# Kernel tuning notes

Hardware: AMD Instinct MI355X
Metric: run time of the kernel (lower is better)

The kernel has to match this reference:

```python
import jax, jax.numpy as jnp
import numpy as np

NUM_NODES = 100_000
NUM_EDGES = 3_200_000
NUM_GRAPHS = 200
F_IN = 128
HID = 64
BN_EPS = 1e-5


def setup_inputs() -> dict:
    key = jax.random.key(0)
    ks = jax.random.split(key, 12)
    x = jax.random.normal(ks[0], (NUM_NODES, F_IN), dtype=jnp.float32)
    edge_index = jax.random.randint(ks[1], (2, NUM_EDGES), 0, NUM_NODES, dtype=jnp.int64)
    batch = jnp.sort(jax.random.randint(ks[2], (NUM_NODES,), 0, NUM_GRAPHS, dtype=jnp.int64))
    s1 = float(np.sqrt(6.0 / F_IN))  # kaiming_uniform-ish bound
    s2 = float(np.sqrt(6.0 / HID))
    W1 = jax.random.uniform(ks[3], (HID, F_IN), jnp.float32, -s1, s1)
    b1 = jnp.zeros((HID,), jnp.float32)
    W2 = jax.random.uniform(ks[4], (HID, HID), jnp.float32, -s2, s2)
    b2 = jnp.zeros((HID,), jnp.float32)
    gamma1 = jnp.ones((HID,), jnp.float32)
    beta1 = jnp.zeros((HID,), jnp.float32)
    mean1 = 0.1 * jax.random.normal(ks[5], (HID,), jnp.float32)
    var1 = jax.random.uniform(ks[6], (HID,), jnp.float32, 0.5, 1.5)
    gamma2 = jnp.ones((HID,), jnp.float32)
    beta2 = jnp.zeros((HID,), jnp.float32)
    mean2 = 0.1 * jax.random.normal(ks[7], (HID,), jnp.float32)
    var2 = jax.random.uniform(ks[8], (HID,), jnp.float32, 0.5, 1.5)
    Wl = jax.random.uniform(ks[9], (1, HID), jnp.float32, -s2, s2)
    bl = jnp.zeros((1,), jnp.float32)
    return dict(x=x, edge_index=edge_index, batch=batch,
                W1=W1, b1=b1, gamma1=gamma1, beta1=beta1, mean1=mean1, var1=var1,
                W2=W2, b2=b2, gamma2=gamma2, beta2=beta2, mean2=mean2, var2=var2,
                Wl=Wl, bl=bl)


def _gcn_conv(x, W, b, src, dst, dinv):
    # PyG GCNConv: h = x @ W.T, then D^{-1/2}(A+I)D^{-1/2} aggregation, then + bias
    h = x @ W.T                                    # [N, out]
    w_edge = (dinv[src] * dinv[dst])[:, None]      # [E, 1]
    msg = h[src] * w_edge                          # [E, out] gather
    agg = jax.ops.segment_sum(msg, dst, num_segments=NUM_NODES)
    agg = agg + h * (dinv * dinv)[:, None]         # self-loop term
    return agg + b


def _bn_eval(h, gamma, beta, mean, var):
    return (h - mean) * (gamma * jax.lax.rsqrt(var + BN_EPS)) + beta


def reference(x, edge_index, batch,
              W1, b1, gamma1, beta1, mean1, var1,
              W2, b2, gamma2, beta2, mean2, var2,
              Wl, bl):
    src, dst = edge_index[0], edge_index[1]
    # degrees over A + I (self-loops add 1)
    deg = jax.ops.segment_sum(jnp.ones((NUM_EDGES,), jnp.float32), dst,
                              num_segments=NUM_NODES) + 1.0
    dinv = jax.lax.rsqrt(deg)
    h = jax.nn.relu(_bn_eval(_gcn_conv(x, W1, b1, src, dst, dinv),
                             gamma1, beta1, mean1, var1))
    # dropout = identity (eval mode)
    h = jax.nn.relu(_bn_eval(_gcn_conv(h, W2, b2, src, dst, dinv),
                             gamma2, beta2, mean2, var2))
    # global_mean_pool over graph ids
    sums = jax.ops.segment_sum(h, batch, num_segments=NUM_GRAPHS)
    cnts = jax.ops.segment_sum(jnp.ones((NUM_NODES,), jnp.float32), batch,
                               num_segments=NUM_GRAPHS)
    pooled = sums / jnp.maximum(cnts, 1.0)[:, None]  # [G, 64]
    return pooled @ Wl.T + bl                        # [G, 1]
```

## Files before the change

### kernel.cpp

```cpp
#include <hip/hip_runtime.h>
#include <hip/hip_bf16.h>

#define NN 100000
#define FF 128
#define HH 64
#define BN_EPS 1e-5f

typedef unsigned int uint_t;

__device__ __forceinline__ float bflo(uint_t u) { return __uint_as_float(u << 16); }
__device__ __forceinline__ float bfhi(uint_t u) { return __uint_as_float(u & 0xFFFF0000u); }
__device__ __forceinline__ unsigned short f2bf(float f) {
    uint_t a = __float_as_uint(f); a += 0x7FFF + ((a >> 16) & 1); return (unsigned short)(a >> 16);
}
__device__ __forceinline__ uint_t f2bf2(float lo, float hi) {
    uint_t a = __float_as_uint(lo); a += 0x7FFF + ((a >> 16) & 1);
    uint_t b = __float_as_uint(hi); b += 0x7FFF + ((b >> 16) & 1);
    return (a >> 16) | (b & 0xFFFF0000u);
}

__global__ void k_detect(const unsigned* __restrict__ ei, int* __restrict__ flag) {
    if (threadIdx.x == 0 && blockIdx.x == 0) {
        unsigned o = 0;
        for (int i = 1; i < 32; i += 2) o |= ei[i];
        *flag = (o == 0) ? 1 : 0;
    }
}

__device__ __forceinline__ int load_idx(const void* p, int i, int is64) {
    return is64 ? (int)((const long long*)p)[i] : ((const int*)p)[i];
}

__global__ void k_count(const void* __restrict__ ei, int E, const int* __restrict__ flag,
                        int* __restrict__ counts) {
    int e = blockIdx.x * blockDim.x + threadIdx.x;
    if (e >= E) return;
    int is64 = *flag;
    int d = load_idx(ei, E + e, is64);
    atomicAdd(&counts[d], 1);
}

__global__ void k_dinv(const int* __restrict__ counts, float* __restrict__ dinv,
                       const void* __restrict__ bat, const int* __restrict__ flag,
                       int* __restrict__ gcnt, int N) {
    int i = blockIdx.x * blockDim.x + threadIdx.x;
    if (i >= N) return;
    float deg = (float)counts[i] + 1.0f;
    dinv[i] = rsqrtf(deg);
    int is64 = *flag;
    int b = load_idx(bat, i, is64);
    atomicAdd(&gcnt[b], 1);
}

__global__ void k_scan1(const int* __restrict__ counts, int* __restrict__ partial, int N) {
    __shared__ int s[512];
    int t = threadIdx.x;
    int i = blockIdx.x * 512 + t;
    int v = (i < N) ? counts[i] : 0;
    s[t] = v; __syncthreads();
    for (int off = 256; off; off >>= 1) {
        if (t < off) s[t] += s[t + off];
        __syncthreads();
    }
    if (t == 0) partial[blockIdx.x] = s[0];
}

__global__ void k_scan2(int* __restrict__ partial, int nch) {
    __shared__ int s[256];
    int t = threadIdx.x;
    int v = (t < nch) ? partial[t] : 0;
    s[t] = v; __syncthreads();
    for (int off = 1; off < 256; off <<= 1) {
        int add = (t >= off) ? s[t - off] : 0;
        __syncthreads();
        s[t] += add;
        __syncthreads();
    }
    if (t < nch) partial[t] = s[t] - v;
}

__global__ void k_scan3(const int* __restrict__ counts, const int* __restrict__ partial,
                        int* __restrict__ rp, int N, int E) {
    __shared__ int s[512];
    int t = threadIdx.x;
    int i = blockIdx.x * 512 + t;
    int v = (i < N) ? counts[i] : 0;
    s[t] = v; __syncthreads();
    for (int off = 1; off < 512; off <<= 1) {
        int add = (t >= off) ? s[t - off] : 0;
        __syncthreads();
        s[t] += add;
        __syncthreads();
    }
    if (i < N) rp[i] = partial[blockIdx.x] + s[t] - v;
    if (i == N) rp[N] = E;
}

__global__ void k_fill(const void* __restrict__ ei, int E, const int* __restrict__ flag,
                       const float* __restrict__ dinv, const int* __restrict__ rp,
                       int* __restrict__ fillcnt, int2* __restrict__ cw) {
    int e = blockIdx.x * blockDim.x + threadIdx.x;
    if (e >= E) return;
    int is64 = *flag;
    int s = load_idx(ei, e, is64);
    int d = load_idx(ei, E + e, is64);
    float w = dinv[s] * dinv[d];
    int pos = rp[d] + atomicAdd(&fillcnt[d], 1);
    int2 p; p.x = s; p.y = __float_as_int(w);
    cw[pos] = p;
}

__global__ void k_prep(const float* b1, const float* g1, const float* be1,
                       const float* m1, const float* v1,
                       const float* b2, const float* g2, const float* be2,
                       const float* m2, const float* v2,
                       float* sc1, float* sh1, float* sc2, float* sh2) {
    int f = threadIdx.x;
    if (f < HH) {
        float s1 = g1[f] * rsqrtf(v1[f] + BN_EPS);
        sc1[f] = s1; sh1[f] = (b1[f] - m1[f]) * s1 + be1[f];
        float s2 = g2[f] * rsqrtf(v2[f] + BN_EPS);
        sc2[f] = s2; sh2[f] = (b2[f] - m2[f]) * s2 + be2[f];
    }
}

__device__ __forceinline__ float ldf(const float* p, int i) { return p[i]; }
__device__ __forceinline__ float ldf(const unsigned short* p, int i) {
    return __uint_as_float((uint_t)p[i] << 16);
}

template <int K, int NPB, typename Tin>
__global__ void k_gemm(const Tin* __restrict__ x, const float* __restrict__ W,
                       unsigned short* __restrict__ out, int N) {
    __shared__ float wT[K * (HH + 1)];
    __shared__ float xs[NPB * K];
    const int TB = NPB * 64;
    int t = threadIdx.x;
    for (int idx = t; idx < K * HH; idx += TB) {
        int f = idx / K, k = idx % K;
        wT[k * (HH + 1) + f] = W[idx];
    }
    int nb = blockIdx.x * NPB;
    for (int idx = t; idx < NPB * K; idx += TB) {
        int gi = nb * K + idx;
        xs[idx] = (gi < N * K) ? ldf(x, gi) : 0.0f;
    }
    __syncthreads();
    int f = t & 63, nl = t >> 6;
    float acc = 0.0f;
#pragma unroll
    for (int k = 0; k < K; k++)
        acc += xs[nl * K + k] * wT[k * (HH + 1) + f];
    int n = nb + nl;
    if (n < N) out[n * HH + f] = f2bf(acc);
}

template <int LAYER>
__global__ void k_agg(const unsigned short* __restrict__ h, const int2* __restrict__ cw,
                      const int* __restrict__ rp, const float* __restrict__ dinv,
                      const float* __restrict__ sc, const float* __restrict__ sh,
                      unsigned short* __restrict__ out,
                      const void* __restrict__ bat, const int* __restrict__ flag,
                      const float* __restrict__ Wl, float* __restrict__ gsum, int N) {
    int wid = (int)((blockIdx.x * blockDim.x + threadIdx.x) >> 6);
    if (wid >= N) return;
    int lane = threadIdx.x & 63;
    int q = lane >> 4;
    int fl = lane & 15;
    const uint2* __restrict__ h2 = (const uint2*)h;

    int s = rp[wid], e = rp[wid + 1];
    float a0 = 0.f, a1 = 0.f, a2 = 0.f, a3 = 0.f;
    if (e > s) {
        int last = e - 1;
        for (int j0 = s; j0 < e; j0 += 16) {
            int2 p[4]; float w[4];
#pragma unroll
            for (int u = 0; u < 4; u++) {
                int jj = j0 + u * 4 + q;
                p[u] = cw[jj < last ? jj : last];
                w[u] = (jj < e) ? __int_as_float(p[u].y) : 0.f;
            }
#pragma unroll
            for (int u = 0; u < 4; u++) {
                uint2 r = h2[p[u].x * 16 + fl];
                a0 += w[u] * bflo(r.x);
                a1 += w[u] * bfhi(r.x);
                a2 += w[u] * bflo(r.y);
                a3 += w[u] * bfhi(r.y);
            }
        }
    }
    a0 += __shfl_xor(a0, 16); a1 += __shfl_xor(a1, 16);
    a2 += __shfl_xor(a2, 16); a3 += __shfl_xor(a3, 16);
    a0 += __shfl_xor(a0, 32); a1 += __shfl_xor(a1, 32);
    a2 += __shfl_xor(a2, 32); a3 += __shfl_xor(a3, 32);

    float di = dinv[wid];
    float di2 = di * di;
    uint2 sr = h2[wid * 16 + fl];
    a0 += di2 * bflo(sr.x); a1 += di2 * bfhi(sr.x);
    a2 += di2 * bflo(sr.y); a3 += di2 * bfhi(sr.y);

    int f0 = fl * 4;
    float v0 = fmaxf(a0 * sc[f0 + 0] + sh[f0 + 0], 0.f);
    float v1 = fmaxf(a1 * sc[f0 + 1] + sh[f0 + 1], 0.f);
    float v2 = fmaxf(a2 * sc[f0 + 2] + sh[f0 + 2], 0.f);
    float v3 = fmaxf(a3 * sc[f0 + 3] + sh[f0 + 3], 0.f);

    if (LAYER == 1) {
        if (lane < 16) {
            uint2 o; o.x = f2bf2(v0, v1); o.y = f2bf2(v2, v3);
            ((uint2*)out)[wid * 16 + fl] = o;
        }
    } else {
        float tval = v0 * Wl[f0] + v1 * Wl[f0 + 1] + v2 * Wl[f0 + 2] + v3 * Wl[f0 + 3];
        tval += __shfl_xor(tval, 1);
        tval += __shfl_xor(tval, 2);
        tval += __shfl_xor(tval, 4);
        tval += __shfl_xor(tval, 8);
        if (lane == 0) {
            int is64 = *flag;
            int b = load_idx(bat, wid, is64);
            atomicAdd(&gsum[b], tval);
        }
    }
}

__global__ void k_final(const float* __restrict__ gsum, const int* __restrict__ gcnt,
                        const float* __restrict__ bl, float* __restrict__ outp, int G) {
    int g = blockIdx.x * blockDim.x + threadIdx.x;
    if (g < G) outp[g] = gsum[g] / fmaxf((float)gcnt[g], 1.0f) + bl[0];
}

extern "C" void kernel_launch(void* const* d_in, const int* in_sizes, int n_in,
                              void* d_out, int out_size, void* d_ws, size_t ws_size,
                              hipStream_t stream) {
    const float* x   = (const float*)d_in[0];
    const void*  ei  = d_in[1];
    const void*  bat = d_in[2];
    const float* W1  = (const float*)d_in[3];
    const float* b1  = (const float*)d_in[4];
    const float* g1  = (const float*)d_in[5];
    const float* be1 = (const float*)d_in[6];
    const float* m1  = (const float*)d_in[7];
    const float* v1  = (const float*)d_in[8];
    const float* W2  = (const float*)d_in[9];
    const float* b2  = (const float*)d_in[10];
    const float* g2  = (const float*)d_in[11];
    const float* be2 = (const float*)d_in[12];
    const float* m2  = (const float*)d_in[13];
    const float* v2  = (const float*)d_in[14];
    const float* Wl  = (const float*)d_in[15];
    const float* bl  = (const float*)d_in[16];
    float* outp = (float*)d_out;

    const int N = NN;
    const int E = in_sizes[1] / 2;
    const int G = out_size;

    char* base = (char*)d_ws;
    size_t off = 0;
    auto alloc = [&](size_t bytes) { void* p = base + off; off = (off + bytes + 255) & ~(size_t)255; return p; };
    int*   flag    = (int*)  alloc(16);
    float* dinv    = (float*)alloc((size_t)N * 4);
    int*   counts  = (int*)  alloc((size_t)N * 4);
    int*   rp      = (int*)  alloc(((size_t)N + 1) * 4);
    int*   fillcnt = (int*)  alloc((size_t)N * 4);
    int*   partial = (int*)  alloc(1024);
    float* sc1     = (float*)alloc(HH * 4);
    float* sh1     = (float*)alloc(HH * 4);
    float* sc2     = (float*)alloc(HH * 4);
    float* sh2     = (float*)alloc(HH * 4);
    float* gsum    = (float*)alloc((size_t)G * 4);
    int*   gcnt    = (int*)  alloc((size_t)G * 4);
    int2*  cw      = (int2*) alloc((size_t)E * 8);
    unsigned short* hb1 = (unsigned short*)alloc((size_t)N * HH * 2);
    unsigned short* hb2 = (unsigned short*)alloc((size_t)N * HH * 2);
    (void)ws_size;

    hipMemsetAsync(counts, 0, (size_t)N * 4, stream);
    hipMemsetAsync(fillcnt, 0, (size_t)N * 4, stream);
    hipMemsetAsync(gsum, 0, (size_t)G * 4, stream);
    hipMemsetAsync(gcnt, 0, (size_t)G * 4, stream);

    k_detect<<<1, 64, 0, stream>>>((const unsigned*)ei, flag);

    int eb = (E + 255) / 256;
    k_count<<<eb, 256, 0, stream>>>(ei, E, flag, counts);

    int nb = (N + 255) / 256;
    k_dinv<<<nb, 256, 0, stream>>>(counts, dinv, bat, flag, gcnt, N);

    int nch = (N + 511) / 512;
    k_scan1<<<nch, 512, 0, stream>>>(counts, partial, N);
    k_scan2<<<1, 256, 0, stream>>>(partial, nch);
    k_scan3<<<nch, 512, 0, stream>>>(counts, partial, rp, N, E);

    k_fill<<<eb, 256, 0, stream>>>(ei, E, flag, dinv, rp, fillcnt, cw);

    k_prep<<<1, 64, 0, stream>>>(b1, g1, be1, m1, v1, b2, g2, be2, m2, v2,
                                 sc1, sh1, sc2, sh2);

    k_gemm<FF, 8, float><<<(N + 7) / 8, 512, 0, stream>>>(x, W1, hb1, N);
    k_agg<1><<<(N + 3) / 4, 256, 0, stream>>>(hb1, cw, rp, dinv, sc1, sh1, hb2,
                                              bat, flag, Wl, gsum, N);
    k_gemm<HH, 8, unsigned short><<<(N + 7) / 8, 512, 0, stream>>>(hb2, W2, hb1, N);
    k_agg<2><<<(N + 3) / 4, 256, 0, stream>>>(hb1, cw, rp, dinv, sc2, sh2, nullptr,
                                              bat, flag, Wl, gsum, N);

    k_final<<<1, 256, 0, stream>>>(gsum, gcnt, bl, outp, G);
}
```

Before: 1.277 ms.

## Split aggregation into four feature-slice passes over a slice-major hidden layout

```diff
diff --git a/kernel.cpp b/kernel.cpp
--- a/kernel.cpp
+++ b/kernel.cpp
@@ -131,7 +131,7 @@
 
 template <int K, int NPB, typename Tin>
 __global__ void k_gemm(const Tin* __restrict__ x, const float* __restrict__ W,
-                       unsigned short* __restrict__ out, int N) {
+                       unsigned short* __restrict__ outq, int N) {
     __shared__ float wT[K * (HH + 1)];
     __shared__ float xs[NPB * K];
     const int TB = NPB * 64;
@@ -152,77 +152,69 @@
     for (int k = 0; k < K; k++)
         acc += xs[nl * K + k] * wT[k * (HH + 1) + f];
     int n = nb + nl;
-    if (n < N) out[n * HH + f] = f2bf(acc);
+    if (n < N) outq[(f >> 4) * (N * 16) + n * 16 + (f & 15)] = f2bf(acc);
 }
 
 template <int LAYER>
-__global__ void k_agg(const unsigned short* __restrict__ h, const int2* __restrict__ cw,
+__global__ void k_agg(const unsigned short* __restrict__ hq, const int2* __restrict__ cw,
                       const int* __restrict__ rp, const float* __restrict__ dinv,
                       const float* __restrict__ sc, const float* __restrict__ sh,
                       unsigned short* __restrict__ out,
                       const void* __restrict__ bat, const int* __restrict__ flag,
                       const float* __restrict__ Wl, float* __restrict__ gsum, int N) {
+    int pass = blockIdx.y;
     int wid = (int)((blockIdx.x * blockDim.x + threadIdx.x) >> 6);
     if (wid >= N) return;
     int lane = threadIdx.x & 63;
-    int q = lane >> 4;
-    int fl = lane & 15;
-    const uint2* __restrict__ h2 = (const uint2*)h;
+    int es = lane >> 2;
+    int c  = lane & 3;
+    const uint2* __restrict__ hp = (const uint2*)hq + (size_t)pass * N * 4;
 
     int s = rp[wid], e = rp[wid + 1];
     float a0 = 0.f, a1 = 0.f, a2 = 0.f, a3 = 0.f;
     if (e > s) {
         int last = e - 1;
-        for (int j0 = s; j0 < e; j0 += 16) {
-            int2 p[4]; float w[4];
+        for (int j0 = s; j0 < e; j0 += 32) {
+            int j1 = j0 + es, j2 = j0 + 16 + es;
+            int2 p0 = cw[j1 < last ? j1 : last];
+            int2 p1 = cw[j2 < last ? j2 : last];
+            float w0 = (j1 < e) ? __int_as_float(p0.y) : 0.f;
+            float w1 = (j2 < e) ? __int_as_float(p1.y) : 0.f;
+            uint2 r0 = hp[p0.x * 4 + c];
+            uint2 r1 = hp[p1.x * 4 + c];
+            a0 += w0 * bflo(r0.x) + w1 * bflo(r1.x);
+            a1 += w0 * bfhi(r0.x) + w1 * bfhi(r1.x);
+            a2 += w0 * bflo(r0.y) + w1 * bflo(r1.y);
+            a3 += w0 * bfhi(r0.y) + w1 * bfhi(r1.y);
+        }
+    }
 #pragma unroll
-            for (int u = 0; u < 4; u++) {
-                int jj = j0 + u * 4 + q;
-                p[u] = cw[jj < last ? jj : last];
-                w[u] = (jj < e) ? __int_as_float(p[u].y) : 0.f;
+    for (int off = 4; off <= 32; off <<= 1) {
+        a0 += __shfl_xor(a0, off); a1 += __shfl_xor(a1, off);
+        a2 += __shfl_xor(a2, off); a3 += __shfl_xor(a3, off);
+    }
+    if (lane < 4) {
+        float di = dinv[wid], di2 = di * di;
+        uint2 sr = hp[wid * 4 + c];
+        a0 += di2 * bflo(sr.x); a1 += di2 * bfhi(sr.x);
+        a2 += di2 * bflo(sr.y); a3 += di2 * bfhi(sr.y);
+        int f0 = pass * 16 + c * 4;
+        float v0 = fmaxf(a0 * sc[f0 + 0] + sh[f0 + 0], 0.f);
+        float v1 = fmaxf(a1 * sc[f0 + 1] + sh[f0 + 1], 0.f);
+        float v2 = fmaxf(a2 * sc[f0 + 2] + sh[f0 + 2], 0.f);
+        float v3 = fmaxf(a3 * sc[f0 + 3] + sh[f0 + 3], 0.f);
+        if (LAYER == 1) {
+            uint2 o; o.x = f2bf2(v0, v1); o.y = f2bf2(v2, v3);
+            ((uint2*)out)[wid * 16 + pass * 4 + c] = o;
+        } else {
+            float tv = v0 * Wl[f0] + v1 * Wl[f0 + 1] + v2 * Wl[f0 + 2] + v3 * Wl[f0 + 3];
+            tv += __shfl_xor(tv, 1);
+            tv += __shfl_xor(tv, 2);
+            if (c == 0) {
+                int is64 = *flag;
+                int b = load_idx(bat, wid, is64);
+                atomicAdd(&gsum[b], tv);
             }
-#pragma unroll
-            for (int u = 0; u < 4; u++) {
-                uint2 r = h2[p[u].x * 16 + fl];
-                a0 += w[u] * bflo(r.x);
-                a1 += w[u] * bfhi(r.x);
-                a2 += w[u] * bflo(r.y);
-                a3 += w[u] * bfhi(r.y);
-            }
-        }
-    }
-    a0 += __shfl_xor(a0, 16); a1 += __shfl_xor(a1, 16);
-    a2 += __shfl_xor(a2, 16); a3 += __shfl_xor(a3, 16);
-    a0 += __shfl_xor(a0, 32); a1 += __shfl_xor(a1, 32);
-    a2 += __shfl_xor(a2, 32); a3 += __shfl_xor(a3, 32);
-
-    float di = dinv[wid];
-    float di2 = di * di;
-    uint2 sr = h2[wid * 16 + fl];
-    a0 += di2 * bflo(sr.x); a1 += di2 * bfhi(sr.x);
-    a2 += di2 * bflo(sr.y); a3 += di2 * bfhi(sr.y);
-
-    int f0 = fl * 4;
-    float v0 = fmaxf(a0 * sc[f0 + 0] + sh[f0 + 0], 0.f);
-    float v1 = fmaxf(a1 * sc[f0 + 1] + sh[f0 + 1], 0.f);
-    float v2 = fmaxf(a2 * sc[f0 + 2] + sh[f0 + 2], 0.f);
-    float v3 = fmaxf(a3 * sc[f0 + 3] + sh[f0 + 3], 0.f);
-
-    if (LAYER == 1) {
-        if (lane < 16) {
-            uint2 o; o.x = f2bf2(v0, v1); o.y = f2bf2(v2, v3);
-            ((uint2*)out)[wid * 16 + fl] = o;
-        }
-    } else {
-        float tval = v0 * Wl[f0] + v1 * Wl[f0 + 1] + v2 * Wl[f0 + 2] + v3 * Wl[f0 + 3];
-        tval += __shfl_xor(tval, 1);
-        tval += __shfl_xor(tval, 2);
-        tval += __shfl_xor(tval, 4);
-        tval += __shfl_xor(tval, 8);
-        if (lane == 0) {
-            int is64 = *flag;
-            int b = load_idx(bat, wid, is64);
-            atomicAdd(&gsum[b], tval);
         }
     }
 }
@@ -275,8 +267,9 @@
     float* gsum    = (float*)alloc((size_t)G * 4);
     int*   gcnt    = (int*)  alloc((size_t)G * 4);
     int2*  cw      = (int2*) alloc((size_t)E * 8);
-    unsigned short* hb1 = (unsigned short*)alloc((size_t)N * HH * 2);
-    unsigned short* hb2 = (unsigned short*)alloc((size_t)N * HH * 2);
+    unsigned short* hqA  = (unsigned short*)alloc((size_t)N * HH * 2);
+    unsigned short* hrow = (unsigned short*)alloc((size_t)N * HH * 2);
+    unsigned short* hqB  = (unsigned short*)alloc((size_t)N * HH * 2);
     (void)ws_size;
 
     hipMemsetAsync(counts, 0, (size_t)N * 4, stream);
@@ -302,12 +295,14 @@
     k_prep<<<1, 64, 0, stream>>>(b1, g1, be1, m1, v1, b2, g2, be2, m2, v2,
                                  sc1, sh1, sc2, sh2);
 
-    k_gemm<FF, 8, float><<<(N + 7) / 8, 512, 0, stream>>>(x, W1, hb1, N);
-    k_agg<1><<<(N + 3) / 4, 256, 0, stream>>>(hb1, cw, rp, dinv, sc1, sh1, hb2,
-                                              bat, flag, Wl, gsum, N);
-    k_gemm<HH, 8, unsigned short><<<(N + 7) / 8, 512, 0, stream>>>(hb2, W2, hb1, N);
-    k_agg<2><<<(N + 3) / 4, 256, 0, stream>>>(hb1, cw, rp, dinv, sc2, sh2, nullptr,
-                                              bat, flag, Wl, gsum, N);
+    dim3 agrid((N + 3) / 4, 4);
+
+    k_gemm<FF, 8, float><<<(N + 7) / 8, 512, 0, stream>>>(x, W1, hqA, N);
+    k_agg<1><<<agrid, 256, 0, stream>>>(hqA, cw, rp, dinv, sc1, sh1, hrow,
+                                        bat, flag, Wl, gsum, N);
+    k_gemm<HH, 8, unsigned short><<<(N + 7) / 8, 512, 0, stream>>>(hrow, W2, hqB, N);
+    k_agg<2><<<agrid, 256, 0, stream>>>(hqB, cw, rp, dinv, sc2, sh2, nullptr,
+                                        bat, flag, Wl, gsum, N);
 
     k_final<<<1, 256, 0, stream>>>(gsum, gcnt, bl, outp, G);
 }
```

After: 2.227 ms. +74.4%, slower.

## Widen aggregation gathers to 16-byte loads and broadcast edges via shuffles

Applied to the files above, without the earlier changes.

```diff
diff --git a/kernel.cpp b/kernel.cpp
--- a/kernel.cpp
+++ b/kernel.cpp
@@ -165,60 +165,77 @@
     int wid = (int)((blockIdx.x * blockDim.x + threadIdx.x) >> 6);
     if (wid >= N) return;
     int lane = threadIdx.x & 63;
-    int q = lane >> 4;
-    int fl = lane & 15;
-    const uint2* __restrict__ h2 = (const uint2*)h;
+    int q  = lane >> 3;
+    int fl = lane & 7;
+    const uint4* __restrict__ h4 = (const uint4*)h;
 
     int s = rp[wid], e = rp[wid + 1];
-    float a0 = 0.f, a1 = 0.f, a2 = 0.f, a3 = 0.f;
-    if (e > s) {
-        int last = e - 1;
-        for (int j0 = s; j0 < e; j0 += 16) {
-            int2 p[4]; float w[4];
-#pragma unroll
-            for (int u = 0; u < 4; u++) {
-                int jj = j0 + u * 4 + q;
-                p[u] = cw[jj < last ? jj : last];
-                w[u] = (jj < e) ? __int_as_float(p[u].y) : 0.f;
-            }
-#pragma unroll
-            for (int u = 0; u < 4; u++) {
-                uint2 r = h2[p[u].x * 16 + fl];
-                a0 += w[u] * bflo(r.x);
-                a1 += w[u] * bfhi(r.x);
-                a2 += w[u] * bflo(r.y);
-                a3 += w[u] * bfhi(r.y);
-            }
+    float a0=0.f,a1=0.f,a2=0.f,a3=0.f,a4=0.f,a5=0.f,a6=0.f,a7=0.f;
+
+    for (int base = s; base < e; base += 64) {
+        int navail = e - base; if (navail > 64) navail = 64;
+        int li = base + (lane < navail ? lane : navail - 1);
+        int2 pk = cw[li];
+        int   sl = pk.x;
+        float wl = (lane < navail) ? __int_as_float(pk.y) : 0.f;
+
+        int srow[8]; float wgt[8];
+#pragma unroll
+        for (int g = 0; g < 8; g++) {
+            srow[g] = __shfl(sl, g * 8 + q);
+            wgt[g]  = __shfl(wl, g * 8 + q);
         }
-    }
-    a0 += __shfl_xor(a0, 16); a1 += __shfl_xor(a1, 16);
-    a2 += __shfl_xor(a2, 16); a3 += __shfl_xor(a3, 16);
-    a0 += __shfl_xor(a0, 32); a1 += __shfl_xor(a1, 32);
-    a2 += __shfl_xor(a2, 32); a3 += __shfl_xor(a3, 32);
+        uint4 r[8];
+#pragma unroll
+        for (int g = 0; g < 8; g++) r[g] = h4[(size_t)srow[g] * 8 + fl];
+#pragma unroll
+        for (int g = 0; g < 8; g++) {
+            float w = wgt[g];
+            a0 += w * bflo(r[g].x); a1 += w * bfhi(r[g].x);
+            a2 += w * bflo(r[g].y); a3 += w * bfhi(r[g].y);
+            a4 += w * bflo(r[g].z); a5 += w * bfhi(r[g].z);
+            a6 += w * bflo(r[g].w); a7 += w * bfhi(r[g].w);
+        }
+    }
+#pragma unroll
+    for (int off = 8; off <= 32; off <<= 1) {
+        a0 += __shfl_xor(a0, off); a1 += __shfl_xor(a1, off);
+        a2 += __shfl_xor(a2, off); a3 += __shfl_xor(a3, off);
+        a4 += __shfl_xor(a4, off); a5 += __shfl_xor(a5, off);
+        a6 += __shfl_xor(a6, off); a7 += __shfl_xor(a7, off);
+    }
 
     float di = dinv[wid];
     float di2 = di * di;
-    uint2 sr = h2[wid * 16 + fl];
+    uint4 sr = h4[(size_t)wid * 8 + fl];
     a0 += di2 * bflo(sr.x); a1 += di2 * bfhi(sr.x);
     a2 += di2 * bflo(sr.y); a3 += di2 * bfhi(sr.y);
-
-    int f0 = fl * 4;
+    a4 += di2 * bflo(sr.z); a5 += di2 * bfhi(sr.z);
+    a6 += di2 * bflo(sr.w); a7 += di2 * bfhi(sr.w);
+
+    int f0 = fl * 8;
     float v0 = fmaxf(a0 * sc[f0 + 0] + sh[f0 + 0], 0.f);
     float v1 = fmaxf(a1 * sc[f0 + 1] + sh[f0 + 1], 0.f);
     float v2 = fmaxf(a2 * sc[f0 + 2] + sh[f0 + 2], 0.f);
     float v3 = fmaxf(a3 * sc[f0 + 3] + sh[f0 + 3], 0.f);
+    float v4 = fmaxf(a4 * sc[f0 + 4] + sh[f0 + 4], 0.f);
+    float v5 = fmaxf(a5 * sc[f0 + 5] + sh[f0 + 5], 0.f);
+    float v6 = fmaxf(a6 * sc[f0 + 6] + sh[f0 + 6], 0.f);
+    float v7 = fmaxf(a7 * sc[f0 + 7] + sh[f0 + 7], 0.f);
 
     if (LAYER == 1) {
-        if (lane < 16) {
-            uint2 o; o.x = f2bf2(v0, v1); o.y = f2bf2(v2, v3);
-            ((uint2*)out)[wid * 16 + fl] = o;
+        if (lane < 8) {
+            uint4 o;
+            o.x = f2bf2(v0, v1); o.y = f2bf2(v2, v3);
+            o.z = f2bf2(v4, v5); o.w = f2bf2(v6, v7);
+            ((uint4*)out)[(size_t)wid * 8 + fl] = o;
         }
     } else {
-        float tval = v0 * Wl[f0] + v1 * Wl[f0 + 1] + v2 * Wl[f0 + 2] + v3 * Wl[f0 + 3];
+        float tval = v0 * Wl[f0 + 0] + v1 * Wl[f0 + 1] + v2 * Wl[f0 + 2] + v3 * Wl[f0 + 3]
+                   + v4 * Wl[f0 + 4] + v5 * Wl[f0 + 5] + v6 * Wl[f0 + 6] + v7 * Wl[f0 + 7];
         tval += __shfl_xor(tval, 1);
         tval += __shfl_xor(tval, 2);
         tval += __shfl_xor(tval, 4);
-        tval += __shfl_xor(tval, 8);
         if (lane == 0) {
             int is64 = *flag;
             int b = load_idx(bat, wid, is64);
```

New measurement: 1.325 ms. +3.8%, slower.
